# Optimization experiments

Hardware: AMD Instinct MI355X
Metric: run time of the kernel (lower is better)

The kernel has to match this reference:

```python
import jax, jax.numpy as jnp
import numpy as np
import math

B, S, D, H, L, F, V, C = 8, 1024, 768, 12, 6, 3072, 32000, 10
DK = D // H
EPS = 1e-5


def _pos_encoding(seq_len, d):
    pos = jnp.arange(seq_len, dtype=jnp.float32)[:, None]
    div = jnp.exp(jnp.arange(0, d, 2, dtype=jnp.float32) * (-math.log(10000.0) / d))
    pe = jnp.zeros((seq_len, d), dtype=jnp.float32)
    pe = pe.at[:, 0::2].set(jnp.sin(pos * div))
    pe = pe.at[:, 1::2].set(jnp.cos(pos * div))
    return pe


def _layernorm(x, scale, bias):
    mu = jnp.mean(x, axis=-1, keepdims=True)
    var = jnp.mean(jnp.square(x - mu), axis=-1, keepdims=True)
    return (x - mu) * jax.lax.rsqrt(var + EPS) * scale + bias


def setup_inputs() -> dict:
    key = jax.random.key(0)
    ks = jax.random.split(key, 14)
    s = 0.02
    return {
        "tokens": jax.random.randint(ks[0], (B, S), 0, V),
        "emb": jax.random.normal(ks[1], (V, D), jnp.float32) * s,
        "Wq": jax.random.normal(ks[2], (L, D, D), jnp.float32) * s,
        "Wk": jax.random.normal(ks[3], (L, D, D), jnp.float32) * s,
        "Wv": jax.random.normal(ks[4], (L, D, D), jnp.float32) * s,
        "Wo": jax.random.normal(ks[5], (L, D, D), jnp.float32) * s,
        "W1": jax.random.normal(ks[6], (L, D, F), jnp.float32) * s,
        "W2": jax.random.normal(ks[7], (L, F, D), jnp.float32) * s,
        "ln1_s": jnp.ones((L, D), jnp.float32),
        "ln1_b": jnp.zeros((L, D), jnp.float32),
        "ln2_s": jnp.ones((L, D), jnp.float32),
        "ln2_b": jnp.zeros((L, D), jnp.float32),
        "Wc": jax.random.normal(ks[8], (D, C), jnp.float32) * s,
        "bc": jnp.zeros((C,), jnp.float32),
    }


def _block(x, p):
    Wq, Wk, Wv, Wo, W1, W2, l1s, l1b, l2s, l2b = p
    b, s = x.shape[0], x.shape[1]
    q = (x @ Wq).reshape(b, s, H, DK)
    k = (x @ Wk).reshape(b, s, H, DK)
    v = (x @ Wv).reshape(b, s, H, DK)
    scores = jnp.einsum("bqhd,bkhd->bhqk", q, k) / math.sqrt(DK)
    attn = jax.nn.softmax(scores, axis=-1)
    out = jnp.einsum("bhqk,bkhd->bqhd", attn, v).reshape(b, s, D) @ Wo
    x = _layernorm(x + out, l1s, l1b)
    ffn = jax.nn.relu(x @ W1) @ W2
    x = _layernorm(x + ffn, l2s, l2b)
    return x


def reference(tokens, emb, Wq, Wk, Wv, Wo, W1, W2, ln1_s, ln1_b, ln2_s, ln2_b, Wc, bc):
    x = emb[tokens] + _pos_encoding(tokens.shape[1], D)[None]

    def step(h, p):
        return _block(h, p), None

    x, _ = jax.lax.scan(step, x, (Wq, Wk, Wv, Wo, W1, W2, ln1_s, ln1_b, ln2_s, ln2_b))
    pooled = jnp.mean(x, axis=1)  # [B, D]
    return pooled @ Wc + bc
```

## Files before the change

### kernel.cpp

```cpp
#include <hip/hip_runtime.h>
#include <hip/hip_bf16.h>
#include <math.h>

#define BB 8
#define SS 1024
#define DD 768
#define HH 12
#define LL 6
#define FF 3072
#define CC 10
#define BS_ (BB * SS)

typedef __attribute__((ext_vector_type(8))) short short8v;
typedef __attribute__((ext_vector_type(4))) float f32x4;
typedef __attribute__((ext_vector_type(16))) float f32x16;
typedef __attribute__((ext_vector_type(8))) unsigned short ushort8v;
typedef __attribute__((ext_vector_type(4))) unsigned short ushort4v;
typedef __attribute__((ext_vector_type(4))) unsigned int uint4v;

__device__ inline unsigned short f2bf(float f) {
  unsigned int u = __builtin_bit_cast(unsigned int, f);
  u += 0x7fffu + ((u >> 16) & 1u);
  return (unsigned short)(u >> 16);
}
__device__ inline float bf2f(unsigned short u) {
  return __builtin_bit_cast(float, (unsigned int)u << 16);
}
__device__ inline unsigned int cvtpk(float lo, float hi) {
  unsigned int r;
  asm("v_cvt_pk_bf16_f32 %0, %1, %2" : "=v"(r) : "v"(lo), "v"(hi));
  return r;
}
__device__ inline void plswap(unsigned int& a, unsigned int& b) {
  asm volatile("v_permlane32_swap_b32 %0, %1" : "+v"(a), "+v"(b));
}
__device__ inline void gload16(const void* g, void* l) {
  __builtin_amdgcn_global_load_lds((const __attribute__((address_space(1))) void*)g,
                                   (__attribute__((address_space(3))) void*)l, 16, 0, 0);
}

__device__ inline float wave_sum(float v) {
#pragma unroll
  for (int off = 32; off > 0; off >>= 1) v += __shfl_down(v, off);
  return v;
}
__device__ inline float block_sum(float v, float* red) {
  int t = threadIdx.x;
  v = wave_sum(v);
  __syncthreads();
  if ((t & 63) == 0) red[t >> 6] = v;
  __syncthreads();
  return red[0] + red[1] + red[2] + red[3];
}

__global__ __launch_bounds__(256) void k_embed(const int* __restrict__ tokens,
                                               const float* __restrict__ emb,
                                               float* __restrict__ x,
                                               ushort* __restrict__ xb) {
  int row = blockIdx.x;
  int s = row & (SS - 1);
  int tok = tokens[row];
  const float* e = emb + (size_t)tok * DD;
  float* xr = x + (size_t)row * DD;
  ushort* xbr = xb + (size_t)row * DD;
  for (int d = threadIdx.x; d < DD; d += 256) {
    float freq = expf((float)(d & ~1) * -0.0119926306f);
    float ang = (float)s * freq;
    float pe = (d & 1) ? cosf(ang) : sinf(ang);
    float v = e[d] + pe;
    xr[d] = v;
    xbr[d] = f2bf(v);
  }
}

__global__ __launch_bounds__(256) void k_transpose_all(
    const float* __restrict__ wq, const float* __restrict__ wk,
    const float* __restrict__ wv, const float* __restrict__ wo,
    const float* __restrict__ w1, const float* __restrict__ w2,
    ushort* __restrict__ wqkv_t, ushort* __restrict__ wo_t,
    ushort* __restrict__ w1_t, ushort* __restrict__ w2_t) {
  __shared__ float tile[32][33];
  int bid = blockIdx.x;
  const float* W; ushort* Wt; int K, N, lb;
  if (bid < 1728) {
    int m = bid / 576; lb = bid - m * 576;
    W = (m == 0) ? wq : (m == 1) ? wk : wv;
    Wt = wqkv_t + m * 768 * 768; K = 768; N = 768;
  } else if (bid < 2304) {
    W = wo; Wt = wo_t; K = 768; N = 768; lb = bid - 1728;
  } else if (bid < 4608) {
    W = w1; Wt = w1_t; K = 768; N = 3072; lb = bid - 2304;
  } else {
    W = w2; Wt = w2_t; K = 3072; N = 768; lb = bid - 4608;
  }
  int nbk = K >> 5;
  int k0 = (lb % nbk) * 32, n0 = (lb / nbk) * 32;
  int t = threadIdx.x;
  int r = t >> 3, c4 = (t & 7) * 4;
  float4 v = *(const float4*)(W + (size_t)(k0 + r) * N + n0 + c4);
  tile[r][c4 + 0] = v.x; tile[r][c4 + 1] = v.y;
  tile[r][c4 + 2] = v.z; tile[r][c4 + 3] = v.w;
  __syncthreads();
  ushort4v o;
#pragma unroll
  for (int i = 0; i < 4; ++i) o[i] = f2bf(tile[c4 + i][r]);
  *(ushort4v*)(Wt + (size_t)(n0 + r) * K + k0 + c4) = o;
}

template <int RELU, int TN>
__global__ __launch_bounds__(256) void k_gemm_db(const ushort* __restrict__ A,
                                                 const ushort* __restrict__ Bt,
                                                 ushort* __restrict__ Cout,
                                                 int M, int N, int K) {
  constexpr int NF = TN / 32;
  __shared__ ushort smem[2][(128 + TN) * 64];
  int bidl = blockIdx.y * gridDim.x + blockIdx.x;
  int nwg = gridDim.x * gridDim.y;
  int cpx = nwg >> 3;
  int tid = (bidl & 7) * cpx + (bidl >> 3);
  int n0 = (tid % gridDim.x) * TN, m0 = (tid / gridDim.x) * 128;
  int t = threadIdx.x, w = t >> 6, l = t & 63;
  int wr = (w >> 1) * 64, wc = (w & 1) * (TN / 2);
  int lr = l & 15, lg = l >> 4;
  f32x4 acc[4][NF] = {};
  int sr8 = l >> 3;
  int scw = ((l & 7) ^ sr8) * 8;
  const ushort* ag = A + (size_t)(m0 + w * 8 + sr8) * K + scw;
  const ushort* bg = Bt + (size_t)(n0 + w * 8 + sr8) * K + scw;
  int nk = K >> 6;
  {
    ushort* al = &smem[0][(w * 8) * 64];
    ushort* bl = &smem[0][128 * 64 + (w * 8) * 64];
#pragma unroll
    for (int ii = 0; ii < 4; ++ii) gload16(ag + (size_t)ii * 32 * K, al + ii * 2048);
#pragma unroll
    for (int ii = 0; ii < TN / 32; ++ii) gload16(bg + (size_t)ii * 32 * K, bl + ii * 2048);
  }
  int rsw = lr & 7;
  for (int k = 0; k < nk; ++k) {
    __syncthreads();
    if (k + 1 < nk) {
      int kb = (k + 1) & 1;
      int kc0 = (k + 1) * 64;
      ushort* al = &smem[kb][(w * 8) * 64];
      ushort* bl = &smem[kb][128 * 64 + (w * 8) * 64];
#pragma unroll
      for (int ii = 0; ii < 4; ++ii) gload16(ag + (size_t)ii * 32 * K + kc0, al + ii * 2048);
#pragma unroll
      for (int ii = 0; ii < TN / 32; ++ii) gload16(bg + (size_t)ii * 32 * K + kc0, bl + ii * 2048);
    }
    const ushort* As = &smem[k & 1][0];
    const ushort* Bs = &smem[k & 1][128 * 64];
#pragma unroll
    for (int ks = 0; ks < 2; ++ks) {
      short8v af[4], bfr[NF];
#pragma unroll
      for (int mi = 0; mi < 4; ++mi)
        af[mi] = *(const short8v*)(As + (wr + mi * 16 + lr) * 64 + (((ks * 4 + lg) ^ rsw) << 3));
#pragma unroll
      for (int ni = 0; ni < NF; ++ni)
        bfr[ni] = *(const short8v*)(Bs + (wc + ni * 16 + lr) * 64 + (((ks * 4 + lg) ^ rsw) << 3));
      __builtin_amdgcn_s_setprio(1);
#pragma unroll
      for (int mi = 0; mi < 4; ++mi)
#pragma unroll
        for (int ni = 0; ni < NF; ++ni)
          acc[mi][ni] = __builtin_amdgcn_mfma_f32_16x16x32_bf16(af[mi], bfr[ni], acc[mi][ni], 0, 0, 0);
      __builtin_amdgcn_s_setprio(0);
    }
  }
  __syncthreads();
  ushort* cst = &smem[0][0];
#pragma unroll
  for (int mi = 0; mi < 4; ++mi)
#pragma unroll
    for (int ni = 0; ni < NF; ++ni) {
      int cl = wc + ni * 16 + lr;
#pragma unroll
      for (int i = 0; i < 4; ++i) {
        int rl = wr + mi * 16 + lg * 4 + i;
        float v = acc[mi][ni][i];
        if (RELU) v = fmaxf(v, 0.f);
        cst[rl * TN + (cl ^ (((rl >> 2) & 3) << 4))] = f2bf(v);
      }
    }
  __syncthreads();
  {
    int row = t >> 1, half = t & 1;
    int swr = ((row >> 2) & 3) << 4;
    ushort* crow = Cout + (size_t)(m0 + row) * N + n0 + half * (TN / 2);
#pragma unroll
    for (int c8 = 0; c8 < TN / 16; ++c8) {
      int c = half * (TN / 2) + c8 * 8;
      ushort8v vv = *(const ushort8v*)(&cst[row * TN + (c ^ swr)]);
      *(ushort8v*)(crow + c8 * 8) = vv;
    }
  }
}

__global__ __launch_bounds__(256) void k_flash(const ushort* __restrict__ qkv,
                                               ushort* __restrict__ ao) {
  __shared__ ushort Ks[2][64][64];
  __shared__ ushort Vt[2][64][64];
  const int LD = 2304;
  int bidl = blockIdx.y * gridDim.x + blockIdx.x;
  int tid = (bidl & 7) * 96 + (bidl >> 3);
  int qt = tid & 7;
  int bh = tid >> 3;
  int hd = bh % HH, b = bh / HH;
  int t = threadIdx.x, w = t >> 6, l = t & 63;
  int q = l & 31, hl = l >> 5;
  int q0 = qt * 128;
  const ushort* qbase = qkv + (size_t)(b * SS) * LD + hd * 64;
  const ushort* kbase = qbase + 768;
  const ushort* vbase = qbase + 1536;
  short8v qfb[4];
  {
    const ushort* qrow = qbase + (size_t)(q0 + w * 32 + q) * LD + hl * 8;
    qfb[0] = *(const short8v*)(qrow);
    qfb[1] = *(const short8v*)(qrow + 16);
    qfb[2] = *(const short8v*)(qrow + 32);
    qfb[3] = *(const short8v*)(qrow + 48);
  }
  const float CEXP = 0.125f * 1.44269504f;
  float l_run = 0.f;
  f32x16 o_acc[2] = {};
  int krow_ = w * 16 + (l >> 3);
  int kcol_ = ((l & 7) * 8) ^ ((krow_ & 7) << 3);
  const ushort* kg = kbase + (size_t)krow_ * LD + kcol_;
  int d_ = t & 7;
  int dk0 = d_ * 8;
  int kv2 = (t >> 3) * 2;
  const ushort* vg = vbase + (size_t)kv2 * LD + dk0;
  {
    gload16(kg, &Ks[0][w * 16][0]);
    gload16(kg + (size_t)8 * LD, &Ks[0][w * 16 + 8][0]);
    ushort8v v0 = *(const ushort8v*)(vg);
    ushort8v v1 = *(const ushort8v*)(vg + LD);
#pragma unroll
    for (int i = 0; i < 8; ++i) {
      unsigned int pk = (unsigned int)v0[i] | ((unsigned int)v1[i] << 16);
      *(unsigned int*)(&Vt[0][dk0 + i][kv2 ^ (((i ^ d_) & 7) << 3)]) = pk;
    }
  }
  for (int kt = 0; kt < 16; ++kt) {
    int cur = kt & 1, nxt = cur ^ 1;
    __syncthreads();
    ushort8v v0n, v1n;
    if (kt < 15) {
      const ushort* kgn = kg + (size_t)(kt + 1) * 64 * LD;
      gload16(kgn, &Ks[nxt][w * 16][0]);
      gload16(kgn + (size_t)8 * LD, &Ks[nxt][w * 16 + 8][0]);
      const ushort* vgn = vg + (size_t)(kt + 1) * 64 * LD;
      v0n = *(const ushort8v*)(vgn);
      v1n = *(const ushort8v*)(vgn + LD);
    }
    f32x16 s[2] = {};
    __builtin_amdgcn_s_setprio(1);
#pragma unroll
    for (int c = 0; c < 4; ++c)
#pragma unroll
      for (int mi = 0; mi < 2; ++mi) {
        short8v kf = *(const short8v*)(
            &Ks[cur][mi * 32 + q][(((c << 1) | hl) ^ (l & 7)) << 3]);
        s[mi] = __builtin_amdgcn_mfma_f32_32x32x16_bf16(kf, qfb[c], s[mi], 0, 0, 0);
      }
    __builtin_amdgcn_s_setprio(0);
    float p[2][16];
    float psum = 0.f;
#pragma unroll
    for (int mi = 0; mi < 2; ++mi)
#pragma unroll
      for (int r = 0; r < 16; ++r) {
        float e = exp2f(s[mi][r] * CEXP);
        p[mi][r] = e;
        psum += e;
      }
    psum += __shfl_xor(psum, 32);
    l_run += psum;
    short8v pfb[4];
#pragma unroll
    for (int mi = 0; mi < 2; ++mi)
#pragma unroll
      for (int k2 = 0; k2 < 2; ++k2) {
        unsigned int a0 = cvtpk(p[mi][8 * k2 + 0], p[mi][8 * k2 + 1]);
        unsigned int a1 = cvtpk(p[mi][8 * k2 + 2], p[mi][8 * k2 + 3]);
        unsigned int b0 = cvtpk(p[mi][8 * k2 + 4], p[mi][8 * k2 + 5]);
        unsigned int b1 = cvtpk(p[mi][8 * k2 + 6], p[mi][8 * k2 + 7]);
        plswap(a0, b0);
        plswap(a1, b1);
        uint4v u;
        u[0] = a0; u[1] = a1; u[2] = b0; u[3] = b1;
        pfb[mi * 2 + k2] = __builtin_bit_cast(short8v, u);
      }
    if (kt < 15) {
#pragma unroll
      for (int i = 0; i < 8; ++i) {
        unsigned int pk = (unsigned int)v0n[i] | ((unsigned int)v1n[i] << 16);
        *(unsigned int*)(&Vt[nxt][dk0 + i][kv2 ^ (((i ^ d_) & 7) << 3)]) = pk;
      }
    }
    __builtin_amdgcn_s_setprio(1);
#pragma unroll
    for (int ks = 0; ks < 4; ++ks)
#pragma unroll
      for (int od = 0; od < 2; ++od) {
        int vsw = ((l & 7) ^ ((od * 4) | ((l >> 3) & 3))) & 7;
        short8v vf = *(const short8v*)(
            &Vt[cur][od * 32 + q][(((ks << 1) | hl) ^ vsw) << 3]);
        o_acc[od] = __builtin_amdgcn_mfma_f32_32x32x16_bf16(vf, pfb[ks], o_acc[od], 0, 0, 0);
      }
    __builtin_amdgcn_s_setprio(0);
  }
  __syncthreads();
  float invl = 1.f / l_run;
  ushort* otile = &Ks[0][0][0] + w * 2048;
#pragma unroll
  for (int od = 0; od < 2; ++od)
#pragma unroll
    for (int r = 0; r < 16; r += 2) {
      unsigned int pk = cvtpk(o_acc[od][r] * invl, o_acc[od][r + 1] * invl);
      int c = od * 32 + 8 * (r >> 2) + 4 * hl + (r & 3);
      *(unsigned int*)(&otile[q * 64 + (c ^ ((q & 7) << 3))]) = pk;
    }
  __syncthreads();
  {
    int r2 = l >> 1, hf = l & 1;
    ushort* orow = ao + (size_t)(b * SS + q0 + w * 32 + r2) * DD + hd * 64 + hf * 32;
#pragma unroll
    for (int k = 0; k < 4; ++k) {
      int c = hf * 32 + k * 8;
      ushort8v vv = *(const ushort8v*)(&otile[r2 * 64 + (c ^ ((r2 & 7) << 3))]);
      *(ushort8v*)(orow + k * 8) = vv;
    }
  }
}

__global__ __launch_bounds__(256) void k_addln(float* __restrict__ x,
                                               ushort* __restrict__ xb,
                                               const ushort* __restrict__ y,
                                               const float* __restrict__ sc,
                                               const float* __restrict__ bi) {
  __shared__ float red[4];
  int row = blockIdx.x, t = threadIdx.x;
  float* xr = x + (size_t)row * DD;
  ushort* xbr = xb + (size_t)row * DD;
  const ushort* yr = y + (size_t)row * DD;
  float vals[3];
  float s = 0.f;
#pragma unroll
  for (int i = 0; i < 3; ++i) {
    float vv = xr[t + 256 * i] + bf2f(yr[t + 256 * i]);
    vals[i] = vv;
    s += vv;
  }
  float mu = block_sum(s, red) * (1.f / 768.f);
  float vs = 0.f;
#pragma unroll
  for (int i = 0; i < 3; ++i) {
    float c = vals[i] - mu;
    vs += c * c;
  }
  float rstd = rsqrtf(block_sum(vs, red) * (1.f / 768.f) + 1e-5f);
#pragma unroll
  for (int i = 0; i < 3; ++i) {
    int d = t + 256 * i;
    float o = (vals[i] - mu) * rstd * sc[d] + bi[d];
    xr[d] = o;
    xbr[d] = f2bf(o);
  }
}

__global__ __launch_bounds__(256) void k_pool(const float* __restrict__ x,
                                              float* __restrict__ pooled) {
  int b = blockIdx.x, chunk = blockIdx.y, t = threadIdx.x;
  float a0 = 0, a1 = 0, a2 = 0;
  for (int s2 = chunk * 128; s2 < chunk * 128 + 128; ++s2) {
    const float* xr = x + (size_t)(b * SS + s2) * DD;
    a0 += xr[t]; a1 += xr[t + 256]; a2 += xr[t + 512];
  }
  atomicAdd(&pooled[b * DD + t], a0 * (1.f / 1024.f));
  atomicAdd(&pooled[b * DD + t + 256], a1 * (1.f / 1024.f));
  atomicAdd(&pooled[b * DD + t + 512], a2 * (1.f / 1024.f));
}

__global__ __launch_bounds__(64) void k_cls(const float* __restrict__ pooled,
                                            const float* __restrict__ Wc,
                                            const float* __restrict__ bc,
                                            float* __restrict__ out) {
  int idx = blockIdx.x;
  int b = idx / CC, c = idx % CC;
  int t = threadIdx.x;
  float acc = 0.f;
  for (int d0 = t; d0 < DD; d0 += 64) acc = fmaf(pooled[b * DD + d0], Wc[d0 * CC + c], acc);
  acc = wave_sum(acc);
  if (t == 0) out[b * CC + c] = acc + bc[c];
}

extern "C" void kernel_launch(void* const* d_in, const int* in_sizes, int n_in,
                              void* d_out, int out_size, void* d_ws, size_t ws_size,
                              hipStream_t stream) {
  (void)in_sizes; (void)n_in; (void)out_size; (void)ws_size;
  const int* tokens = (const int*)d_in[0];
  const float* emb = (const float*)d_in[1];
  const float* Wq = (const float*)d_in[2];
  const float* Wk = (const float*)d_in[3];
  const float* Wv = (const float*)d_in[4];
  const float* Wo = (const float*)d_in[5];
  const float* W1 = (const float*)d_in[6];
  const float* W2 = (const float*)d_in[7];
  const float* l1s = (const float*)d_in[8];
  const float* l1b = (const float*)d_in[9];
  const float* l2s = (const float*)d_in[10];
  const float* l2b = (const float*)d_in[11];
  const float* Wc = (const float*)d_in[12];
  const float* bc = (const float*)d_in[13];
  float* out = (float*)d_out;

  char* p = (char*)d_ws;
  float* x = (float*)p;                 p += (size_t)BS_ * DD * 4;
  ushort* xb = (ushort*)p;              p += (size_t)BS_ * DD * 2;
  ushort* qkvb = (ushort*)p;
  ushort* hb = (ushort*)p;
  ushort* ao = (ushort*)(p + (size_t)BS_ * 2304 * 2);
  p += (size_t)BS_ * FF * 2;
  ushort* yb = (ushort*)p;              p += (size_t)BS_ * DD * 2;
  ushort* wt = (ushort*)p;              p += (size_t)(2304 * 768 + 768 * 768 + 3072 * 768 + 768 * 3072) * 2;
  float* pooled = (float*)p;

  ushort* wqkv_t = wt;
  ushort* wo_t = wqkv_t + 2304 * 768;
  ushort* w1_t = wo_t + 768 * 768;
  ushort* w2_t = w1_t + 3072 * 768;

  k_embed<<<BS_, 256, 0, stream>>>(tokens, emb, x, xb);

  for (int l = 0; l < LL; ++l) {
    k_transpose_all<<<6912, 256, 0, stream>>>(
        Wq + (size_t)l * DD * DD, Wk + (size_t)l * DD * DD,
        Wv + (size_t)l * DD * DD, Wo + (size_t)l * DD * DD,
        W1 + (size_t)l * DD * FF, W2 + (size_t)l * FF * DD,
        wqkv_t, wo_t, w1_t, w2_t);

    k_gemm_db<0, 128><<<dim3(2304 / 128, BS_ / 128), 256, 0, stream>>>(xb, wqkv_t, qkvb, BS_, 2304, DD);
    k_flash<<<dim3(SS / 128, BB * HH), 256, 0, stream>>>(qkvb, ao);
    k_gemm_db<0, 64><<<dim3(DD / 64, BS_ / 128), 256, 0, stream>>>(ao, wo_t, yb, BS_, DD, DD);
    k_addln<<<BS_, 256, 0, stream>>>(x, xb, yb, l1s + l * DD, l1b + l * DD);
    k_gemm_db<1, 128><<<dim3(FF / 128, BS_ / 128), 256, 0, stream>>>(xb, w1_t, hb, BS_, FF, DD);
    k_gemm_db<0, 64><<<dim3(DD / 64, BS_ / 128), 256, 0, stream>>>(hb, w2_t, yb, BS_, DD, FF);
    k_addln<<<BS_, 256, 0, stream>>>(x, xb, yb, l2s + l * DD, l2b + l * DD);
  }

  hipMemsetAsync(pooled, 0, (size_t)BB * DD * sizeof(float), stream);
  k_pool<<<dim3(BB, 8), 256, 0, stream>>>(x, pooled);
  k_cls<<<BB * CC, 64, 0, stream>>>(pooled, Wc, bc, out);
}
```

Measured before the change: 1.527 ms.

## Drop fp32 residual stream, use single-wave bf16 add-layernorm, reswizzle flash K tile

Removes the fp32 copy of the residual stream x. Embedding, residual add, layernorm and pooling now read and write only the bf16 activations, which cuts memory traffic in the add-layernorm and pool kernels. The add-layernorm kernel becomes one 64-thread wave per row with vector loads and shuffle reductions, so it no longer needs shared-memory block reductions. The flash attention K tile gets an extra XOR swizzle term to reduce LDS bank conflicts, and the probability array reuses the score registers. Keeping the residual in bf16 across all layers lowers accuracy.

```diff
diff --git a/kernel.cpp b/kernel.cpp
--- a/kernel.cpp
+++ b/kernel.cpp
@@ -44,32 +44,20 @@
   for (int off = 32; off > 0; off >>= 1) v += __shfl_down(v, off);
   return v;
 }
-__device__ inline float block_sum(float v, float* red) {
-  int t = threadIdx.x;
-  v = wave_sum(v);
-  __syncthreads();
-  if ((t & 63) == 0) red[t >> 6] = v;
-  __syncthreads();
-  return red[0] + red[1] + red[2] + red[3];
-}
 
 __global__ __launch_bounds__(256) void k_embed(const int* __restrict__ tokens,
                                                const float* __restrict__ emb,
-                                               float* __restrict__ x,
                                                ushort* __restrict__ xb) {
   int row = blockIdx.x;
   int s = row & (SS - 1);
   int tok = tokens[row];
   const float* e = emb + (size_t)tok * DD;
-  float* xr = x + (size_t)row * DD;
   ushort* xbr = xb + (size_t)row * DD;
   for (int d = threadIdx.x; d < DD; d += 256) {
     float freq = expf((float)(d & ~1) * -0.0119926306f);
     float ang = (float)s * freq;
     float pe = (d & 1) ? cosf(ang) : sinf(ang);
-    float v = e[d] + pe;
-    xr[d] = v;
-    xbr[d] = f2bf(v);
+    xbr[d] = f2bf(e[d] + pe);
   }
 }
 
@@ -225,16 +213,18 @@
   const float CEXP = 0.125f * 1.44269504f;
   float l_run = 0.f;
   f32x16 o_acc[2] = {};
-  int krow_ = w * 16 + (l >> 3);
-  int kcol_ = ((l & 7) * 8) ^ ((krow_ & 7) << 3);
-  const ushort* kg = kbase + (size_t)krow_ * LD + kcol_;
+  int r8_ = l >> 3;
+  const ushort* kgA = kbase + (size_t)(w * 16 + r8_) * LD +
+                      (((l & 7) ^ r8_ ^ ((2 * w) & 3)) * 8);
+  const ushort* kgB = kbase + (size_t)(w * 16 + 8 + r8_) * LD +
+                      (((l & 7) ^ r8_ ^ ((2 * w + 1) & 3)) * 8);
   int d_ = t & 7;
   int dk0 = d_ * 8;
   int kv2 = (t >> 3) * 2;
   const ushort* vg = vbase + (size_t)kv2 * LD + dk0;
   {
-    gload16(kg, &Ks[0][w * 16][0]);
-    gload16(kg + (size_t)8 * LD, &Ks[0][w * 16 + 8][0]);
+    gload16(kgA, &Ks[0][w * 16][0]);
+    gload16(kgB, &Ks[0][w * 16 + 8][0]);
     ushort8v v0 = *(const ushort8v*)(vg);
     ushort8v v1 = *(const ushort8v*)(vg + LD);
 #pragma unroll
@@ -248,10 +238,10 @@
     __syncthreads();
     ushort8v v0n, v1n;
     if (kt < 15) {
-      const ushort* kgn = kg + (size_t)(kt + 1) * 64 * LD;
-      gload16(kgn, &Ks[nxt][w * 16][0]);
-      gload16(kgn + (size_t)8 * LD, &Ks[nxt][w * 16 + 8][0]);
-      const ushort* vgn = vg + (size_t)(kt + 1) * 64 * LD;
+      size_t off = (size_t)(kt + 1) * 64 * LD;
+      gload16(kgA + off, &Ks[nxt][w * 16][0]);
+      gload16(kgB + off, &Ks[nxt][w * 16 + 8][0]);
+      const ushort* vgn = vg + off;
       v0n = *(const ushort8v*)(vgn);
       v1n = *(const ushort8v*)(vgn + LD);
     }
@@ -261,19 +251,18 @@
     for (int c = 0; c < 4; ++c)
 #pragma unroll
       for (int mi = 0; mi < 2; ++mi) {
-        short8v kf = *(const short8v*)(
-            &Ks[cur][mi * 32 + q][(((c << 1) | hl) ^ (l & 7)) << 3]);
+        int gr = ((c << 1) | hl) ^ (l & 7) ^ ((l >> 3) & 3);
+        short8v kf = *(const short8v*)(&Ks[cur][mi * 32 + q][gr << 3]);
         s[mi] = __builtin_amdgcn_mfma_f32_32x32x16_bf16(kf, qfb[c], s[mi], 0, 0, 0);
       }
     __builtin_amdgcn_s_setprio(0);
-    float p[2][16];
     float psum = 0.f;
 #pragma unroll
     for (int mi = 0; mi < 2; ++mi)
 #pragma unroll
       for (int r = 0; r < 16; ++r) {
         float e = exp2f(s[mi][r] * CEXP);
-        p[mi][r] = e;
+        s[mi][r] = e;
         psum += e;
       }
     psum += __shfl_xor(psum, 32);
@@ -283,10 +272,10 @@
     for (int mi = 0; mi < 2; ++mi)
 #pragma unroll
       for (int k2 = 0; k2 < 2; ++k2) {
-        unsigned int a0 = cvtpk(p[mi][8 * k2 + 0], p[mi][8 * k2 + 1]);
-        unsigned int a1 = cvtpk(p[mi][8 * k2 + 2], p[mi][8 * k2 + 3]);
-        unsigned int b0 = cvtpk(p[mi][8 * k2 + 4], p[mi][8 * k2 + 5]);
-        unsigned int b1 = cvtpk(p[mi][8 * k2 + 6], p[mi][8 * k2 + 7]);
+        unsigned int a0 = cvtpk(s[mi][8 * k2 + 0], s[mi][8 * k2 + 1]);
+        unsigned int a1 = cvtpk(s[mi][8 * k2 + 2], s[mi][8 * k2 + 3]);
+        unsigned int b0 = cvtpk(s[mi][8 * k2 + 4], s[mi][8 * k2 + 5]);
+        unsigned int b1 = cvtpk(s[mi][8 * k2 + 6], s[mi][8 * k2 + 7]);
         plswap(a0, b0);
         plswap(a1, b1);
         uint4v u;
@@ -336,48 +325,64 @@
   }
 }
 
-__global__ __launch_bounds__(256) void k_addln(float* __restrict__ x,
-                                               ushort* __restrict__ xb,
-                                               const ushort* __restrict__ y,
-                                               const float* __restrict__ sc,
-                                               const float* __restrict__ bi) {
-  __shared__ float red[4];
-  int row = blockIdx.x, t = threadIdx.x;
-  float* xr = x + (size_t)row * DD;
-  ushort* xbr = xb + (size_t)row * DD;
+__global__ __launch_bounds__(64) void k_addln(ushort* __restrict__ xb,
+                                              const ushort* __restrict__ y,
+                                              const float* __restrict__ sc,
+                                              const float* __restrict__ bi) {
+  int row = blockIdx.x, l = threadIdx.x;
+  int d0 = l * 12;
+  ushort* xr = xb + (size_t)row * DD;
   const ushort* yr = y + (size_t)row * DD;
-  float vals[3];
+  ushort4v xa[3], ya[3];
+#pragma unroll
+  for (int j = 0; j < 3; ++j) {
+    xa[j] = *(const ushort4v*)(xr + d0 + j * 4);
+    ya[j] = *(const ushort4v*)(yr + d0 + j * 4);
+  }
+  float v[12];
   float s = 0.f;
 #pragma unroll
-  for (int i = 0; i < 3; ++i) {
-    float vv = xr[t + 256 * i] + bf2f(yr[t + 256 * i]);
-    vals[i] = vv;
-    s += vv;
-  }
-  float mu = block_sum(s, red) * (1.f / 768.f);
+  for (int j = 0; j < 3; ++j)
+#pragma unroll
+    for (int i = 0; i < 4; ++i) {
+      float vv = bf2f(xa[j][i]) + bf2f(ya[j][i]);
+      v[j * 4 + i] = vv;
+      s += vv;
+    }
+  float mu = wave_sum(s);
+  mu = __shfl(mu, 0) * (1.f / 768.f);
   float vs = 0.f;
 #pragma unroll
-  for (int i = 0; i < 3; ++i) {
-    float c = vals[i] - mu;
+  for (int i = 0; i < 12; ++i) {
+    float c = v[i] - mu;
     vs += c * c;
   }
-  float rstd = rsqrtf(block_sum(vs, red) * (1.f / 768.f) + 1e-5f);
-#pragma unroll
-  for (int i = 0; i < 3; ++i) {
-    int d = t + 256 * i;
-    float o = (vals[i] - mu) * rstd * sc[d] + bi[d];
-    xr[d] = o;
-    xbr[d] = f2bf(o);
-  }
-}
-
-__global__ __launch_bounds__(256) void k_pool(const float* __restrict__ x,
+  vs = wave_sum(vs);
+  float rstd = rsqrtf(__shfl(vs, 0) * (1.f / 768.f) + 1e-5f);
+  float4 scv[3], biv[3];
+#pragma unroll
+  for (int j = 0; j < 3; ++j) {
+    scv[j] = *(const float4*)(sc + d0 + j * 4);
+    biv[j] = *(const float4*)(bi + d0 + j * 4);
+  }
+#pragma unroll
+  for (int j = 0; j < 3; ++j) {
+    ushort4v o;
+    const float* sj = (const float*)&scv[j];
+    const float* bj = (const float*)&biv[j];
+#pragma unroll
+    for (int i = 0; i < 4; ++i) o[i] = f2bf((v[j * 4 + i] - mu) * rstd * sj[i] + bj[i]);
+    *(ushort4v*)(xr + d0 + j * 4) = o;
+  }
+}
+
+__global__ __launch_bounds__(256) void k_pool(const ushort* __restrict__ xb,
                                               float* __restrict__ pooled) {
   int b = blockIdx.x, chunk = blockIdx.y, t = threadIdx.x;
   float a0 = 0, a1 = 0, a2 = 0;
   for (int s2 = chunk * 128; s2 < chunk * 128 + 128; ++s2) {
-    const float* xr = x + (size_t)(b * SS + s2) * DD;
-    a0 += xr[t]; a1 += xr[t + 256]; a2 += xr[t + 512];
+    const ushort* xr = xb + (size_t)(b * SS + s2) * DD;
+    a0 += bf2f(xr[t]); a1 += bf2f(xr[t + 256]); a2 += bf2f(xr[t + 512]);
   }
   atomicAdd(&pooled[b * DD + t], a0 * (1.f / 1024.f));
   atomicAdd(&pooled[b * DD + t + 256], a1 * (1.f / 1024.f));
@@ -418,7 +423,6 @@
   float* out = (float*)d_out;
 
   char* p = (char*)d_ws;
-  float* x = (float*)p;                 p += (size_t)BS_ * DD * 4;
   ushort* xb = (ushort*)p;              p += (size_t)BS_ * DD * 2;
   ushort* qkvb = (ushort*)p;
   ushort* hb = (ushort*)p;
@@ -433,7 +437,7 @@
   ushort* w1_t = wo_t + 768 * 768;
   ushort* w2_t = w1_t + 3072 * 768;
 
-  k_embed<<<BS_, 256, 0, stream>>>(tokens, emb, x, xb);
+  k_embed<<<BS_, 256, 0, stream>>>(tokens, emb, xb);
 
   for (int l = 0; l < LL; ++l) {
     k_transpose_all<<<6912, 256, 0, stream>>>(
@@ -445,13 +449,13 @@
     k_gemm_db<0, 128><<<dim3(2304 / 128, BS_ / 128), 256, 0, stream>>>(xb, wqkv_t, qkvb, BS_, 2304, DD);
     k_flash<<<dim3(SS / 128, BB * HH), 256, 0, stream>>>(qkvb, ao);
     k_gemm_db<0, 64><<<dim3(DD / 64, BS_ / 128), 256, 0, stream>>>(ao, wo_t, yb, BS_, DD, DD);
-    k_addln<<<BS_, 256, 0, stream>>>(x, xb, yb, l1s + l * DD, l1b + l * DD);
+    k_addln<<<BS_, 64, 0, stream>>>(xb, yb, l1s + l * DD, l1b + l * DD);
     k_gemm_db<1, 128><<<dim3(FF / 128, BS_ / 128), 256, 0, stream>>>(xb, w1_t, hb, BS_, FF, DD);
     k_gemm_db<0, 64><<<dim3(DD / 64, BS_ / 128), 256, 0, stream>>>(hb, w2_t, yb, BS_, DD, FF);
-    k_addln<<<BS_, 256, 0, stream>>>(x, xb, yb, l2s + l * DD, l2b + l * DD);
+    k_addln<<<BS_, 64, 0, stream>>>(xb, yb, l2s + l * DD, l2b + l * DD);
   }
 
   hipMemsetAsync(pooled, 0, (size_t)BB * DD * sizeof(float), stream);
-  k_pool<<<dim3(BB, 8), 256, 0, stream>>>(x, pooled);
+  k_pool<<<dim3(BB, 8), 256, 0, stream>>>(xb, pooled);
   k_cls<<<BB * CC, 64, 0, stream>>>(pooled, Wc, bc, out);
 }
```

Result: faster. 1.448 ms (-5.2%).
